# Kernel optimization log

Hardware: AMD Instinct MI355X
Metric: run time of the kernel (lower is better)

The kernel has to match this reference:

```python
import jax, jax.numpy as jnp
import numpy as np

S = 1024      # flattened hierarchical sequence length
D = 1024      # n_embd
H = 16        # n_head
HD = D // H   # head dim (64)
NL = 6        # n_layer
DFF = 4 * D
EPS = 1.1920929e-07  # torch rms_norm default eps (float32 machine eps)


def setup_inputs() -> dict:
    key = jax.random.key(0)
    ks = jax.random.split(key, 12)
    s = 0.02
    return {
        "x": jax.random.normal(ks[0], (1, S, D), jnp.float32),
        "Wq": jax.random.normal(ks[1], (NL, D, D), jnp.float32) * s,
        "Wk": jax.random.normal(ks[2], (NL, D, D), jnp.float32) * s,
        "Wv": jax.random.normal(ks[3], (NL, D, D), jnp.float32) * s,
        "Wo": jax.random.normal(ks[4], (NL, D, D), jnp.float32) * s,
        "lamb": jnp.full((NL,), 0.5, jnp.float32),
        "lambdas": jnp.tile(jnp.array([1.0, 0.0], jnp.float32), (NL, 1)),
        "Wfc": jax.random.normal(ks[5], (NL, DFF, D), jnp.float32) * s,
        "Wp": jax.random.normal(ks[6], (NL, D, DFF), jnp.float32) * s,
        "levels": jax.random.randint(ks[7], (S,), 0, 3, jnp.int32),
        "sample_idx": jnp.sort(jax.random.randint(ks[8], (S,), 0, 8, jnp.int32)),
    }


def rms(t):
    return t * jax.lax.rsqrt(jnp.mean(t * t, axis=-1, keepdims=True) + EPS)


def rope(t):
    # t: [B, T, H, hd]; torch-style half-split rotary
    hd = t.shape[-1]
    d = hd // 2
    inv = 1.0 / (10000.0 ** (jnp.arange(0, hd, 2, dtype=jnp.float32) / hd))
    fr = jnp.outer(jnp.arange(t.shape[1], dtype=jnp.float32), inv)  # [T, d]
    cos = jnp.cos(fr)[None, :, None, :]
    sin = jnp.sin(fr)[None, :, None, :]
    x1, x2 = t[..., :d], t[..., d:]
    return jnp.concatenate([x1 * cos + x2 * sin, -x1 * sin + x2 * cos], axis=-1)


def markov_mask(levels, sample_idx):
    # allowed(q,kv) = causal & same-sample & NOT(levels[kv]==0 and a level-0
    # token exists strictly between kv and q). Equivalent to the torch
    # markov_causal_mask, computed via a cumsum instead of torch.any.
    n = levels.shape[0]
    pos = jnp.arange(n)
    causal = pos[:, None] >= pos[None, :]
    same = sample_idx[:, None] == sample_idx[None, :]
    c = jnp.cumsum((levels == 0).astype(jnp.int32))
    cpad = jnp.concatenate([jnp.zeros((1,), jnp.int32), c])  # cpad[i]=#l0 in [0,i)
    # count of level-0 tokens at positions p with kv < p < q
    cnt = cpad[pos[:, None]] - cpad[pos[None, :] + 1]
    markov = (levels[None, :] == 0) & (cnt > 0)
    return causal & same & ~markov


def reference(x, Wq, Wk, Wv, Wo, lamb, lambdas, Wfc, Wp, levels, sample_idx):
    mask = markov_mask(levels, sample_idx)[None, None]  # [1,1,S,S]
    scale = HD ** -0.5
    neg = jnp.float32(-1e30)

    x = rms(x)          # norm of the hierarchical-trajectory embedding
    x0 = x
    v1 = None
    for i in range(NL):
        xl = lambdas[i, 0] * x + lambdas[i, 1] * x0
        xn = rms(xl)
        B, T = xn.shape[0], xn.shape[1]
        q = (xn @ Wq[i].T).reshape(B, T, H, HD)
        k = (xn @ Wk[i].T).reshape(B, T, H, HD)
        v = (xn @ Wv[i].T).reshape(B, T, H, HD)
        if v1 is None:
            v1 = v
        v = (1.0 - lamb[i]) * v + lamb[i] * v1   # value residual
        q, k = rms(q), rms(k)                    # QK RMSNorm
        q, k = rope(q), rope(k)
        scores = jnp.einsum("bqhd,bkhd->bhqk", q, k) * scale
        scores = jnp.where(mask, scores, neg)
        p = jax.nn.softmax(scores, axis=-1)
        y = jnp.einsum("bhqk,bkhd->bqhd", p, v).reshape(B, T, D)
        x = xl + y @ Wo[i].T
        h = rms(x) @ Wfc[i].T
        h = jnp.square(jax.nn.relu(h))           # relu(x)^2 activation
        x = x + h @ Wp[i].T
    return rms(x)
```

## Files before the change

### kernel.cpp

```cpp
#include <hip/hip_runtime.h>

#define SQ 1024
#define DM 1024
#define NH 16
#define HD 64
#define NL 6
#define DFF 4096
#define EPS 1.1920929e-07f

typedef __attribute__((ext_vector_type(8))) short short8;
typedef __attribute__((ext_vector_type(4))) float floatx4;
typedef __attribute__((address_space(1))) const unsigned int GU32;
typedef __attribute__((address_space(3))) unsigned int LU32;

__device__ __forceinline__ unsigned short f2b(float f) {
    union { float f; unsigned int u; } x; x.f = f;
    unsigned int r = x.u + 0x7fffu + ((x.u >> 16) & 1u);
    return (unsigned short)(r >> 16);
}

__device__ __forceinline__ float wsum(float v) {
#pragma unroll
    for (int m = 32; m >= 1; m >>= 1) v += __shfl_xor(v, m, 64);
    return v;
}
__device__ __forceinline__ float bsum(float v) {
    __shared__ float sh[4];
    v = wsum(v);
    __syncthreads();
    if ((threadIdx.x & 63) == 0) sh[threadIdx.x >> 6] = v;
    __syncthreads();
    return sh[0] + sh[1] + sh[2] + sh[3];
}

__global__ void convert_all(const float* __restrict__ s0, const float* __restrict__ s1,
                            const float* __restrict__ s2, const float* __restrict__ s3,
                            const float* __restrict__ s4, const float* __restrict__ s5,
                            unsigned short* __restrict__ d0, unsigned short* __restrict__ d1,
                            unsigned short* __restrict__ d2, unsigned short* __restrict__ d3,
                            unsigned short* __restrict__ d4, unsigned short* __restrict__ d5) {
    int bid = blockIdx.x;
    const float* src; unsigned short* dst; long base;
    if (bid < 3072)        { src = s0; dst = d0; base = (long)bid * 512; }
    else if (bid < 6144)   { src = s1; dst = d1; base = (long)(bid - 3072) * 512; }
    else if (bid < 9216)   { src = s2; dst = d2; base = (long)(bid - 6144) * 512; }
    else if (bid < 12288)  { src = s3; dst = d3; base = (long)(bid - 9216) * 512; }
    else if (bid < 24576)  { src = s4; dst = d4; base = (long)(bid - 12288) * 512; }
    else                   { src = s5; dst = d5; base = (long)(bid - 24576) * 512; }
    long i0 = base + threadIdx.x;
#pragma unroll
    for (int u = 0; u < 2; ++u) {
        long i = i0 + u * 256;
        float4 v = ((const float4*)src)[i];
        ushort4 o;
        o.x = f2b(v.x); o.y = f2b(v.y); o.z = f2b(v.z); o.w = f2b(v.w);
        ((ushort4*)dst)[i] = o;
    }
}

__global__ void build_rope(float2* __restrict__ tab) {
    int i = blockIdx.x * 256 + threadIdx.x;
    int s = i >> 5, d = i & 31;
    float invf = expf(-((float)(2 * d) / (float)HD) * 9.210340371976184f);
    float fr = (float)s * invf;
    tab[i] = make_float2(cosf(fr), sinf(fr));
}

__global__ void scan_levels(const int* __restrict__ levels, int* __restrict__ cpad) {
    __shared__ int sh[SQ];
    int t = threadIdx.x;
    sh[t] = (levels[t] == 0) ? 1 : 0;
    __syncthreads();
    for (int off = 1; off < SQ; off <<= 1) {
        int v = (t >= off) ? sh[t - off] : 0;
        __syncthreads();
        sh[t] += v;
        __syncthreads();
    }
    cpad[t + 1] = sh[t];
    if (t == 0) cpad[0] = 0;
}

__global__ void build_mask_bits(const int* __restrict__ levels, const int* __restrict__ sidx,
                                const int* __restrict__ cpad, unsigned long long* __restrict__ mb) {
    int i = blockIdx.x * 256 + threadIdx.x;
    int q = i >> 10, k = i & 1023;
    bool causal = q >= k;
    bool same = sidx[q] == sidx[k];
    int cnt = cpad[q] - cpad[k + 1];
    bool markov = (levels[k] == 0) && (cnt > 0);
    bool pred = causal && same && !markov;
    unsigned long long bal = __ballot(pred);
    if ((threadIdx.x & 63) == 0) mb[(size_t)q * 16 + (k >> 6)] = bal;
}

__global__ void rms0(const float* __restrict__ xin, const float* __restrict__ lam2,
                     float* __restrict__ x0, float* __restrict__ xl,
                     unsigned short* __restrict__ xnb) {
    int row = blockIdx.x, t = threadIdx.x;
    float l0 = lam2[0], l1 = lam2[1];
    const float* rp = xin + (size_t)row * DM;
    float v[4]; float ss = 0.f;
#pragma unroll
    for (int j = 0; j < 4; ++j) { v[j] = rp[t + j * 256]; ss += v[j] * v[j]; }
    ss = bsum(ss);
    float inv = rsqrtf(ss / (float)DM + EPS);
    float coef = l0 + l1;
    float w[4]; float ss2 = 0.f;
#pragma unroll
    for (int j = 0; j < 4; ++j) {
        float r = v[j] * inv;
        x0[(size_t)row * DM + t + j * 256] = r;
        w[j] = coef * r;
        ss2 += w[j] * w[j];
    }
    ss2 = bsum(ss2);
    float inv2 = rsqrtf(ss2 / (float)DM + EPS);
#pragma unroll
    for (int j = 0; j < 4; ++j) {
        size_t idx = (size_t)row * DM + t + j * 256;
        xl[idx] = w[j];
        xnb[idx] = f2b(w[j] * inv2);
    }
}

__global__ __launch_bounds__(256, 2)
void gemm_qkv(const unsigned short* __restrict__ A,
              const unsigned short* __restrict__ B0,
              long long sB,
              unsigned short* __restrict__ qb, unsigned short* __restrict__ kb,
              float* __restrict__ vf,
              const float2* __restrict__ rope) {
    constexpr int BM = 64, BN = 128, BK = 32;
    __shared__ unsigned short As[BM * BK];
    __shared__ unsigned short Bs[BN * BK];
    int t = threadIdx.x, wave = t >> 6, lane = t & 63;
    int m0 = blockIdx.y * BM, n0 = blockIdx.x * BN;
    int z = blockIdx.z;
    const unsigned short* Bb = B0 + (size_t)z * sB;
    int r = lane & 15, q4 = lane >> 4;
    int sr = lane >> 2, sseg = lane & 3;
    int wmo = (wave >> 1) * 32, wno = (wave & 1) * 64;

    floatx4 acc[2][4] = {};
    for (int k0 = 0; k0 < DM; k0 += BK) {
        {
            int c = wave;
            const unsigned short* g = A + (size_t)(m0 + c * 16 + sr) * DM + k0 + sseg * 8;
            __builtin_amdgcn_global_load_lds((GU32*)g, (LU32*)(As + c * 512), 16, 0, 0);
        }
#pragma unroll
        for (int j = 0; j < 2; ++j) {
            int c = wave * 2 + j;
            const unsigned short* g = Bb + (size_t)(n0 + c * 16 + sr) * DM + k0 + sseg * 8;
            __builtin_amdgcn_global_load_lds((GU32*)g, (LU32*)(Bs + c * 512), 16, 0, 0);
        }
        __syncthreads();
        short8 af[2], bfr[4];
#pragma unroll
        for (int mi = 0; mi < 2; ++mi)
            af[mi] = *(const short8*)(As + (wmo + mi * 16 + r) * BK + q4 * 8);
#pragma unroll
        for (int ni = 0; ni < 4; ++ni)
            bfr[ni] = *(const short8*)(Bs + (wno + ni * 16 + r) * BK + q4 * 8);
#pragma unroll
        for (int mi = 0; mi < 2; ++mi)
#pragma unroll
            for (int ni = 0; ni < 4; ++ni)
                acc[mi][ni] = __builtin_amdgcn_mfma_f32_16x16x32_bf16(af[mi], bfr[ni], acc[mi][ni], 0, 0, 0);
        __syncthreads();
    }

    if (z == 2) {
#pragma unroll
        for (int mi = 0; mi < 2; ++mi)
#pragma unroll
            for (int ni = 0; ni < 4; ++ni)
#pragma unroll
                for (int j = 0; j < 4; ++j)
                    vf[(size_t)(m0 + wmo + mi * 16 + q4 * 4 + j) * DM + n0 + wno + ni * 16 + r] = acc[mi][ni][j];
        return;
    }
    unsigned short* dst = z ? kb : qb;
#pragma unroll
    for (int mi = 0; mi < 2; ++mi) {
#pragma unroll
        for (int j = 0; j < 4; ++j) {
            int row = m0 + wmo + mi * 16 + q4 * 4 + j;
            float v0 = acc[mi][0][j], v1 = acc[mi][1][j], v2 = acc[mi][2][j], v3 = acc[mi][3][j];
            float ss = v0 * v0 + v1 * v1 + v2 * v2 + v3 * v3;
#pragma unroll
            for (int d = 1; d < 16; d <<= 1) ss += __shfl_xor(ss, d, 64);
            float inv = rsqrtf(ss * (1.f / 64.f) + EPS);
            v0 *= inv; v1 *= inv; v2 *= inv; v3 *= inv;
            float2 t0 = rope[row * 32 + r];
            float2 t1 = rope[row * 32 + 16 + r];
            size_t rb = (size_t)row * DM + n0 + wno + r;
            dst[rb]      = f2b(v0 * t0.x + v2 * t0.y);
            dst[rb + 16] = f2b(v1 * t1.x + v3 * t1.y);
            dst[rb + 32] = f2b(v2 * t0.x - v0 * t0.y);
            dst[rb + 48] = f2b(v3 * t1.x - v1 * t1.y);
        }
    }
}

__global__ void v_post(const float* __restrict__ vf, float* __restrict__ v1,
                       unsigned short* __restrict__ vt, const float* __restrict__ lambp,
                       int first) {
    __shared__ unsigned short tile[64 * 65];
    int b = blockIdx.x;
    int t = threadIdx.x;
    int ts = b >> 4, tc = b & 15;
    float l = lambp[0];
#pragma unroll
    for (int j = 0; j < 16; ++j) {
        int idx = j * 256 + t;
        int s = idx >> 6, c = idx & 63;
        size_t gi = (size_t)(ts * 64 + s) * DM + tc * 64 + c;
        float val = vf[gi];
        float v1v;
        if (first) { v1[gi] = val; v1v = val; } else v1v = v1[gi];
        tile[c * 65 + s] = f2b((1.f - l) * val + l * v1v);
    }
    __syncthreads();
#pragma unroll
    for (int j = 0; j < 16; ++j) {
        int idx = j * 256 + t;
        int c = idx >> 6, s = idx & 63;
        vt[(size_t)(tc * 64 + c) * SQ + ts * 64 + s] = tile[c * 65 + s];
    }
}

__global__ __launch_bounds__(64)
void flash_attn(const unsigned short* __restrict__ qb, const unsigned short* __restrict__ kb,
                const unsigned short* __restrict__ vt, const unsigned long long* __restrict__ mb,
                unsigned short* __restrict__ yb) {
    __shared__ unsigned short Ps[16 * 64];
    int lane = threadIdx.x;
    int qt = blockIdx.x & 63, h = blockIdx.x >> 6;
    int q0 = qt * 16;
    int r = lane & 15, q4 = lane >> 4;
    const unsigned short* qp = qb + (size_t)(q0 + r) * DM + h * HD + q4 * 8;
    short8 aq0 = *(const short8*)qp;
    short8 aq1 = *(const short8*)(qp + 32);
    floatx4 o[4] = {};
    float m[4] = {-1e30f, -1e30f, -1e30f, -1e30f};
    float l[4] = {0.f, 0.f, 0.f, 0.f};
    int nk = (qt >> 2) + 1;
    for (int kt = 0; kt < nk; ++kt) {
        int k0 = kt * 64;
        unsigned long long mw[4];
#pragma unroll
        for (int j = 0; j < 4; ++j) mw[j] = mb[(size_t)(q0 + q4 * 4 + j) * 16 + kt];
        unsigned long long any = mw[0] | mw[1] | mw[2] | mw[3];
        if (__ballot(any != 0ull) == 0ull) continue;
        short8 bk[4][2], bv[4][2];
#pragma unroll
        for (int ni = 0; ni < 4; ++ni) {
            const unsigned short* kp = kb + (size_t)(k0 + ni * 16 + r) * DM + h * HD + q4 * 8;
            bk[ni][0] = *(const short8*)kp;
            bk[ni][1] = *(const short8*)(kp + 32);
            const unsigned short* vp = vt + (size_t)(h * HD + ni * 16 + r) * SQ + k0 + q4 * 8;
            bv[ni][0] = *(const short8*)vp;
            bv[ni][1] = *(const short8*)(vp + 32);
        }
        float sm[4][4];
#pragma unroll
        for (int ni = 0; ni < 4; ++ni) {
            floatx4 z = {};
            z = __builtin_amdgcn_mfma_f32_16x16x32_bf16(aq0, bk[ni][0], z, 0, 0, 0);
            z = __builtin_amdgcn_mfma_f32_16x16x32_bf16(aq1, bk[ni][1], z, 0, 0, 0);
#pragma unroll
            for (int j = 0; j < 4; ++j) {
                float sv = z[j] * 0.125f;
                bool bit = (mw[j] >> (ni * 16 + r)) & 1ull;
                sm[ni][j] = bit ? sv : -__builtin_inff();
            }
        }
        float alpha[4];
#pragma unroll
        for (int j = 0; j < 4; ++j) {
            float v = fmaxf(fmaxf(sm[0][j], sm[1][j]), fmaxf(sm[2][j], sm[3][j]));
#pragma unroll
            for (int d = 1; d < 16; d <<= 1) v = fmaxf(v, __shfl_xor(v, d, 64));
            float mn = fmaxf(m[j], v);
            alpha[j] = __expf(m[j] - mn);
            m[j] = mn;
        }
        float p[4][4];
        float rs[4] = {0.f, 0.f, 0.f, 0.f};
#pragma unroll
        for (int ni = 0; ni < 4; ++ni)
#pragma unroll
            for (int j = 0; j < 4; ++j) {
                p[ni][j] = __expf(sm[ni][j] - m[j]);
                rs[j] += p[ni][j];
            }
#pragma unroll
        for (int j = 0; j < 4; ++j) {
            float v = rs[j];
#pragma unroll
            for (int d = 1; d < 16; d <<= 1) v += __shfl_xor(v, d, 64);
            l[j] = l[j] * alpha[j] + v;
        }
#pragma unroll
        for (int ni = 0; ni < 4; ++ni)
#pragma unroll
            for (int j = 0; j < 4; ++j) {
                o[ni][j] *= alpha[j];
                Ps[(q4 * 4 + j) * 64 + ni * 16 + r] = f2b(p[ni][j]);
            }
        short8 ap0 = *(const short8*)(Ps + r * 64 + q4 * 8);
        short8 ap1 = *(const short8*)(Ps + r * 64 + 32 + q4 * 8);
#pragma unroll
        for (int ni = 0; ni < 4; ++ni) {
            o[ni] = __builtin_amdgcn_mfma_f32_16x16x32_bf16(ap0, bv[ni][0], o[ni], 0, 0, 0);
            o[ni] = __builtin_amdgcn_mfma_f32_16x16x32_bf16(ap1, bv[ni][1], o[ni], 0, 0, 0);
        }
    }
#pragma unroll
    for (int j = 0; j < 4; ++j) l[j] = 1.f / l[j];
#pragma unroll
    for (int ni = 0; ni < 4; ++ni)
#pragma unroll
        for (int j = 0; j < 4; ++j)
            yb[(size_t)(q0 + q4 * 4 + j) * DM + h * HD + ni * 16 + r] = f2b(o[ni][j] * l[j]);
}

template<int BM, int BN>
__global__ __launch_bounds__(256, 2)
void gemm_t(const unsigned short* __restrict__ A, int lda, long long sA,
            const unsigned short* __restrict__ B, int ldb, long long sB,
            float* Cf, unsigned short* Cb, int ldc, long long sC,
            const float* __restrict__ addsrc, int ldadd,
            int K, float scale, int act) {
    constexpr int BK = 32;
    constexpr int MI = BM / 32, NI = BN / 32;
    constexpr int CA = BM / 16, CB = BN / 16;
    constexpr int CAW = CA / 4, CBW = CB / 4;
    __shared__ unsigned short As[BM * BK];
    __shared__ unsigned short Bs[BN * BK];

    int t = threadIdx.x;
    int wave = t >> 6, lane = t & 63;
    int m0 = blockIdx.y * BM, n0 = blockIdx.x * BN;
    int z = blockIdx.z;
    const unsigned short* Ab = A + (size_t)z * sA;
    const unsigned short* Bb = B + (size_t)z * sB;

    int r = lane & 15, q4 = lane >> 4;
    int sr = lane >> 2, sseg = lane & 3;
    int wmo = (wave >> 1) * (BM / 2);
    int wno = (wave & 1) * (BN / 2);

    floatx4 acc[MI][NI] = {};

    for (int k0 = 0; k0 < K; k0 += BK) {
#pragma unroll
        for (int j = 0; j < CAW; ++j) {
            int c = wave * CAW + j;
            const unsigned short* g = Ab + (size_t)(m0 + c * 16 + sr) * lda + k0 + sseg * 8;
            __builtin_amdgcn_global_load_lds((GU32*)g, (LU32*)(As + c * 512), 16, 0, 0);
        }
#pragma unroll
        for (int j = 0; j < CBW; ++j) {
            int c = wave * CBW + j;
            const unsigned short* g = Bb + (size_t)(n0 + c * 16 + sr) * ldb + k0 + sseg * 8;
            __builtin_amdgcn_global_load_lds((GU32*)g, (LU32*)(Bs + c * 512), 16, 0, 0);
        }
        __syncthreads();

        short8 af[MI], bfr[NI];
#pragma unroll
        for (int mi = 0; mi < MI; ++mi)
            af[mi] = *(const short8*)(As + (wmo + mi * 16 + r) * BK + q4 * 8);
#pragma unroll
        for (int ni = 0; ni < NI; ++ni)
            bfr[ni] = *(const short8*)(Bs + (wno + ni * 16 + r) * BK + q4 * 8);
#pragma unroll
        for (int mi = 0; mi < MI; ++mi)
#pragma unroll
            for (int ni = 0; ni < NI; ++ni)
                acc[mi][ni] = __builtin_amdgcn_mfma_f32_16x16x32_bf16(af[mi], bfr[ni], acc[mi][ni], 0, 0, 0);
        __syncthreads();
    }

    size_t cz = (size_t)z * sC;
#pragma unroll
    for (int mi = 0; mi < MI; ++mi) {
#pragma unroll
        for (int ni = 0; ni < NI; ++ni) {
            int col = n0 + wno + ni * 16 + r;
#pragma unroll
            for (int j = 0; j < 4; ++j) {
                int row = m0 + wmo + mi * 16 + q4 * 4 + j;
                float v = acc[mi][ni][j] * scale;
                if (addsrc) v += addsrc[(size_t)row * ldadd + col];
                if (act == 1) { v = fmaxf(v, 0.f); v = v * v; }
                if (Cf) Cf[cz + (size_t)row * ldc + col] = v;
                if (Cb) Cb[cz + (size_t)row * ldc + col] = f2b(v);
            }
        }
    }
}

__global__ void wo_rms(const float* __restrict__ xl, const float* __restrict__ pp,
                       float* __restrict__ x, unsigned short* __restrict__ xhb) {
    int row = blockIdx.x, t = threadIdx.x;
    const long n = (long)SQ * DM;
    size_t base = (size_t)row * DM;
    float a[4]; float ss = 0.f;
#pragma unroll
    for (int j = 0; j < 4; ++j) {
        size_t idx = base + t + j * 256;
        float v = xl[idx] + pp[idx] + pp[idx + n];
        x[idx] = v;
        a[j] = v; ss += v * v;
    }
    ss = bsum(ss);
    float inv = rsqrtf(ss / (float)DM + EPS);
#pragma unroll
    for (int j = 0; j < 4; ++j)
        xhb[base + t + j * 256] = f2b(a[j] * inv);
}

__global__ void proj_reduce_xlrms(const float* __restrict__ x, const float* __restrict__ pp,
                                  const float* __restrict__ x0, const float* __restrict__ lam2,
                                  float* __restrict__ xl, unsigned short* __restrict__ xnb,
                                  float* __restrict__ out, int last) {
    int row = blockIdx.x, t = threadIdx.x;
    const long n = (long)SQ * DM;
    size_t base = (size_t)row * DM;
    float l0 = 0.f, l1 = 0.f;
    if (!last) { l0 = lam2[0]; l1 = lam2[1]; }
    float a[4]; float ss = 0.f;
#pragma unroll
    for (int j = 0; j < 4; ++j) {
        size_t idx = base + t + j * 256;
        float v = x[idx] + pp[idx] + pp[idx + n] + pp[idx + 2 * n] + pp[idx + 3 * n];
        if (!last) { v = l0 * v + l1 * x0[idx]; xl[idx] = v; }
        a[j] = v; ss += v * v;
    }
    ss = bsum(ss);
    float inv = rsqrtf(ss / (float)DM + EPS);
#pragma unroll
    for (int j = 0; j < 4; ++j) {
        size_t idx = base + t + j * 256;
        if (last) out[idx] = a[j] * inv;
        else xnb[idx] = f2b(a[j] * inv);
    }
}

extern "C" void kernel_launch(void* const* d_in, const int* in_sizes, int n_in,
                              void* d_out, int out_size, void* d_ws, size_t ws_size,
                              hipStream_t stream) {
    const float* x_in    = (const float*)d_in[0];
    const float* Wq      = (const float*)d_in[1];
    const float* Wk      = (const float*)d_in[2];
    const float* Wv      = (const float*)d_in[3];
    const float* Wo      = (const float*)d_in[4];
    const float* lamb    = (const float*)d_in[5];
    const float* lambdas = (const float*)d_in[6];
    const float* Wfc     = (const float*)d_in[7];
    const float* Wp      = (const float*)d_in[8];
    const int*   levels  = (const int*)d_in[9];
    const int*   sidx    = (const int*)d_in[10];
    float* out = (float*)d_out;

    char* ws = (char*)d_ws;
    size_t off = 0;
    auto alloc = [&](size_t b) { void* p = ws + off; off = (off + b + 255) & ~(size_t)255; return p; };

    unsigned short* wq_b  = (unsigned short*)alloc((size_t)NL * DM * DM * 2);
    unsigned short* wk_b  = (unsigned short*)alloc((size_t)NL * DM * DM * 2);
    unsigned short* wv_b  = (unsigned short*)alloc((size_t)NL * DM * DM * 2);
    unsigned short* wo_b  = (unsigned short*)alloc((size_t)NL * DM * DM * 2);
    unsigned short* wfc_b = (unsigned short*)alloc((size_t)NL * DFF * DM * 2);
    unsigned short* wp_b  = (unsigned short*)alloc((size_t)NL * DM * DFF * 2);
    int* cpad             = (int*)alloc((SQ + 1) * 4);
    unsigned long long* mb = (unsigned long long*)alloc((size_t)SQ * 16 * 8);
    float2* rope          = (float2*)alloc((size_t)SQ * 32 * 8);
    float* x    = (float*)alloc((size_t)SQ * DM * 4);
    float* x0   = (float*)alloc((size_t)SQ * DM * 4);
    float* xl   = (float*)alloc((size_t)SQ * DM * 4);
    float* vf   = (float*)alloc((size_t)SQ * DM * 4);
    float* v1   = (float*)alloc((size_t)SQ * DM * 4);
    float* pp   = (float*)alloc((size_t)4 * SQ * DM * 4);
    unsigned short* xn_b = (unsigned short*)alloc((size_t)SQ * DM * 2);
    unsigned short* qb   = (unsigned short*)alloc((size_t)SQ * DM * 2);
    unsigned short* kb   = (unsigned short*)alloc((size_t)SQ * DM * 2);
    unsigned short* vt   = (unsigned short*)alloc((size_t)SQ * DM * 2);
    unsigned short* y_b  = (unsigned short*)alloc((size_t)SQ * DM * 2);
    unsigned short* xh_b = (unsigned short*)alloc((size_t)SQ * DM * 2);
    unsigned short* h_b  = (unsigned short*)alloc((size_t)SQ * DFF * 2);

    if (off > ws_size) return;

    const long long WSTRIDE = (long long)NL * DM * DM;
    const long long XSTRIDE = (long long)SQ * DM;

    convert_all<<<36864, 256, 0, stream>>>(Wq, Wk, Wv, Wo, Wfc, Wp,
                                           wq_b, wk_b, wv_b, wo_b, wfc_b, wp_b);

    scan_levels<<<1, 1024, 0, stream>>>(levels, cpad);
    build_mask_bits<<<4096, 256, 0, stream>>>(levels, sidx, cpad, mb);
    build_rope<<<128, 256, 0, stream>>>(rope);

    rms0<<<SQ, 256, 0, stream>>>(x_in, lambdas, x0, xl, xn_b);

    for (int i = 0; i < NL; ++i) {
        gemm_qkv<<<dim3(8, 16, 3), 256, 0, stream>>>(
            xn_b, wq_b + (size_t)i * DM * DM, WSTRIDE, qb, kb, vf, rope);

        v_post<<<256, 256, 0, stream>>>(vf, v1, vt, lamb + i, (i == 0) ? 1 : 0);

        flash_attn<<<1024, 64, 0, stream>>>(qb, kb, vt, mb, y_b);

        gemm_t<64, 64><<<dim3(16, 16, 2), 256, 0, stream>>>(
            y_b, DM, 512, wo_b + (size_t)i * DM * DM, DM, 512,
            pp, nullptr, DM, XSTRIDE, nullptr, 0, 512, 1.f, 0);
        wo_rms<<<SQ, 256, 0, stream>>>(xl, pp, x, xh_b);

        gemm_t<128, 64><<<dim3(64, 8, 1), 256, 0, stream>>>(
            xh_b, DM, 0, wfc_b + (size_t)i * DFF * DM, DM, 0,
            nullptr, h_b, DFF, 0, nullptr, 0, DM, 1.f, 1);
        gemm_t<128, 64><<<dim3(16, 8, 4), 256, 0, stream>>>(
            h_b, DFF, 1024, wp_b + (size_t)i * DM * DFF, DFF, 1024,
            pp, nullptr, DM, XSTRIDE, nullptr, 0, 1024, 1.f, 0);
        proj_reduce_xlrms<<<SQ, 256, 0, stream>>>(
            x, pp, x0, (i < NL - 1) ? (lambdas + 2 * (i + 1)) : nullptr,
            xl, xn_b, out, (i == NL - 1) ? 1 : 0);
    }
}
```

Measured before the change: 1.027 ms.

## Double-buffer GEMM LDS tiles, fuse value post-processing into QKV GEMM, widen conversion

Both GEMM kernels now double-buffer their LDS tiles, so the global-to-LDS load for the next K step is issued before the MFMAs on the current tile. This is meant to overlap memory latency with compute and removes one barrier per iteration. The separate v_post kernel is folded into the QKV GEMM epilogue, which applies the value residual and transposes through an LDS tile, removing the fp32 vf round trip and one launch per layer. The weight conversion kernel also handles 8 elements per thread with 16-byte stores. In exchange, LDS use per block roughly doubles, which may lower occupancy.

New measurement: 1.061 ms. 1.03x slower.

```diff
diff --git a/kernel.cpp b/kernel.cpp
--- a/kernel.cpp
+++ b/kernel.cpp
@@ -41,20 +41,24 @@
                             unsigned short* __restrict__ d4, unsigned short* __restrict__ d5) {
     int bid = blockIdx.x;
     const float* src; unsigned short* dst; long base;
-    if (bid < 3072)        { src = s0; dst = d0; base = (long)bid * 512; }
-    else if (bid < 6144)   { src = s1; dst = d1; base = (long)(bid - 3072) * 512; }
-    else if (bid < 9216)   { src = s2; dst = d2; base = (long)(bid - 6144) * 512; }
-    else if (bid < 12288)  { src = s3; dst = d3; base = (long)(bid - 9216) * 512; }
-    else if (bid < 24576)  { src = s4; dst = d4; base = (long)(bid - 12288) * 512; }
-    else                   { src = s5; dst = d5; base = (long)(bid - 24576) * 512; }
+    if (bid < 1536)        { src = s0; dst = d0; base = (long)bid * 512; }
+    else if (bid < 3072)   { src = s1; dst = d1; base = (long)(bid - 1536) * 512; }
+    else if (bid < 4608)   { src = s2; dst = d2; base = (long)(bid - 3072) * 512; }
+    else if (bid < 6144)   { src = s3; dst = d3; base = (long)(bid - 4608) * 512; }
+    else if (bid < 12288)  { src = s4; dst = d4; base = (long)(bid - 6144) * 512; }
+    else                   { src = s5; dst = d5; base = (long)(bid - 12288) * 512; }
     long i0 = base + threadIdx.x;
 #pragma unroll
     for (int u = 0; u < 2; ++u) {
         long i = i0 + u * 256;
-        float4 v = ((const float4*)src)[i];
-        ushort4 o;
-        o.x = f2b(v.x); o.y = f2b(v.y); o.z = f2b(v.z); o.w = f2b(v.w);
-        ((ushort4*)dst)[i] = o;
+        float4 a = ((const float4*)src)[2 * i];
+        float4 b = ((const float4*)src)[2 * i + 1];
+        short8 o;
+        o[0] = (short)f2b(a.x); o[1] = (short)f2b(a.y);
+        o[2] = (short)f2b(a.z); o[3] = (short)f2b(a.w);
+        o[4] = (short)f2b(b.x); o[5] = (short)f2b(b.y);
+        o[6] = (short)f2b(b.z); o[7] = (short)f2b(b.w);
+        *(short8*)(dst + i * 8) = o;
     }
 }
 
@@ -129,11 +133,13 @@
               const unsigned short* __restrict__ B0,
               long long sB,
               unsigned short* __restrict__ qb, unsigned short* __restrict__ kb,
-              float* __restrict__ vf,
-              const float2* __restrict__ rope) {
+              float* __restrict__ v1, unsigned short* __restrict__ vt,
+              const float2* __restrict__ rope,
+              const float* __restrict__ lambp, int first) {
     constexpr int BM = 64, BN = 128, BK = 32;
-    __shared__ unsigned short As[BM * BK];
-    __shared__ unsigned short Bs[BN * BK];
+    __shared__ unsigned short As[2][BM * BK];
+    __shared__ unsigned short Bs[2][BN * BK];
+    __shared__ unsigned short vtile[128 * 72];
     int t = threadIdx.x, wave = t >> 6, lane = t & 63;
     int m0 = blockIdx.y * BM, n0 = blockIdx.x * BN;
     int z = blockIdx.z;
@@ -143,91 +149,98 @@
     int wmo = (wave >> 1) * 32, wno = (wave & 1) * 64;
 
     floatx4 acc[2][4] = {};
+
+    {
+        const unsigned short* g = A + (size_t)(m0 + wave * 16 + sr) * DM + sseg * 8;
+        __builtin_amdgcn_global_load_lds((GU32*)g, (LU32*)(&As[0][wave * 512]), 16, 0, 0);
+    }
+#pragma unroll
+    for (int j = 0; j < 2; ++j) {
+        int c = wave * 2 + j;
+        const unsigned short* g = Bb + (size_t)(n0 + c * 16 + sr) * DM + sseg * 8;
+        __builtin_amdgcn_global_load_lds((GU32*)g, (LU32*)(&Bs[0][c * 512]), 16, 0, 0);
+    }
+    __syncthreads();
+
+    int cur = 0;
     for (int k0 = 0; k0 < DM; k0 += BK) {
-        {
-            int c = wave;
-            const unsigned short* g = A + (size_t)(m0 + c * 16 + sr) * DM + k0 + sseg * 8;
-            __builtin_amdgcn_global_load_lds((GU32*)g, (LU32*)(As + c * 512), 16, 0, 0);
-        }
-#pragma unroll
-        for (int j = 0; j < 2; ++j) {
-            int c = wave * 2 + j;
-            const unsigned short* g = Bb + (size_t)(n0 + c * 16 + sr) * DM + k0 + sseg * 8;
-            __builtin_amdgcn_global_load_lds((GU32*)g, (LU32*)(Bs + c * 512), 16, 0, 0);
-        }
-        __syncthreads();
+        int kn = k0 + BK;
+        if (kn < DM) {
+            {
+                const unsigned short* g = A + (size_t)(m0 + wave * 16 + sr) * DM + kn + sseg * 8;
+                __builtin_amdgcn_global_load_lds((GU32*)g, (LU32*)(&As[cur ^ 1][wave * 512]), 16, 0, 0);
+            }
+#pragma unroll
+            for (int j = 0; j < 2; ++j) {
+                int c = wave * 2 + j;
+                const unsigned short* g = Bb + (size_t)(n0 + c * 16 + sr) * DM + kn + sseg * 8;
+                __builtin_amdgcn_global_load_lds((GU32*)g, (LU32*)(&Bs[cur ^ 1][c * 512]), 16, 0, 0);
+            }
+        }
         short8 af[2], bfr[4];
 #pragma unroll
         for (int mi = 0; mi < 2; ++mi)
-            af[mi] = *(const short8*)(As + (wmo + mi * 16 + r) * BK + q4 * 8);
+            af[mi] = *(const short8*)(&As[cur][(wmo + mi * 16 + r) * BK + q4 * 8]);
 #pragma unroll
         for (int ni = 0; ni < 4; ++ni)
-            bfr[ni] = *(const short8*)(Bs + (wno + ni * 16 + r) * BK + q4 * 8);
+            bfr[ni] = *(const short8*)(&Bs[cur][(wno + ni * 16 + r) * BK + q4 * 8]);
 #pragma unroll
         for (int mi = 0; mi < 2; ++mi)
 #pragma unroll
             for (int ni = 0; ni < 4; ++ni)
                 acc[mi][ni] = __builtin_amdgcn_mfma_f32_16x16x32_bf16(af[mi], bfr[ni], acc[mi][ni], 0, 0, 0);
         __syncthreads();
+        cur ^= 1;
     }
 
     if (z == 2) {
+        float l = lambp[0];
 #pragma unroll
         for (int mi = 0; mi < 2; ++mi)
 #pragma unroll
             for (int ni = 0; ni < 4; ++ni)
 #pragma unroll
-                for (int j = 0; j < 4; ++j)
-                    vf[(size_t)(m0 + wmo + mi * 16 + q4 * 4 + j) * DM + n0 + wno + ni * 16 + r] = acc[mi][ni][j];
+                for (int j = 0; j < 4; ++j) {
+                    int row = m0 + wmo + mi * 16 + q4 * 4 + j;
+                    int col = n0 + wno + ni * 16 + r;
+                    float val = acc[mi][ni][j];
+                    size_t gi = (size_t)row * DM + col;
+                    float v1v;
+                    if (first) { v1[gi] = val; v1v = val; } else v1v = v1[gi];
+                    vtile[(col - n0) * 72 + (row - m0)] = f2b((1.f - l) * val + l * v1v);
+                }
+        __syncthreads();
+#pragma unroll
+        for (int jj = 0; jj < 4; ++jj) {
+            int idx = jj * 256 + t;
+            int cr = idx >> 3;
+            int seg = idx & 7;
+            short8 o = *(const short8*)(&vtile[cr * 72 + seg * 8]);
+            *(short8*)(vt + (size_t)(n0 + cr) * SQ + m0 + seg * 8) = o;
+        }
         return;
     }
+
     unsigned short* dst = z ? kb : qb;
 #pragma unroll
     for (int mi = 0; mi < 2; ++mi) {
 #pragma unroll
         for (int j = 0; j < 4; ++j) {
             int row = m0 + wmo + mi * 16 + q4 * 4 + j;
-            float v0 = acc[mi][0][j], v1 = acc[mi][1][j], v2 = acc[mi][2][j], v3 = acc[mi][3][j];
-            float ss = v0 * v0 + v1 * v1 + v2 * v2 + v3 * v3;
+            float v0 = acc[mi][0][j], v1x = acc[mi][1][j], v2 = acc[mi][2][j], v3 = acc[mi][3][j];
+            float ss = v0 * v0 + v1x * v1x + v2 * v2 + v3 * v3;
 #pragma unroll
             for (int d = 1; d < 16; d <<= 1) ss += __shfl_xor(ss, d, 64);
             float inv = rsqrtf(ss * (1.f / 64.f) + EPS);
-            v0 *= inv; v1 *= inv; v2 *= inv; v3 *= inv;
+            v0 *= inv; v1x *= inv; v2 *= inv; v3 *= inv;
             float2 t0 = rope[row * 32 + r];
             float2 t1 = rope[row * 32 + 16 + r];
             size_t rb = (size_t)row * DM + n0 + wno + r;
             dst[rb]      = f2b(v0 * t0.x + v2 * t0.y);
-            dst[rb + 16] = f2b(v1 * t1.x + v3 * t1.y);
+            dst[rb + 16] = f2b(v1x * t1.x + v3 * t1.y);
             dst[rb + 32] = f2b(v2 * t0.x - v0 * t0.y);
-            dst[rb + 48] = f2b(v3 * t1.x - v1 * t1.y);
-        }
-    }
-}
-
-__global__ void v_post(const float* __restrict__ vf, float* __restrict__ v1,
-                       unsigned short* __restrict__ vt, const float* __restrict__ lambp,
-                       int first) {
-    __shared__ unsigned short tile[64 * 65];
-    int b = blockIdx.x;
-    int t = threadIdx.x;
-    int ts = b >> 4, tc = b & 15;
-    float l = lambp[0];
-#pragma unroll
-    for (int j = 0; j < 16; ++j) {
-        int idx = j * 256 + t;
-        int s = idx >> 6, c = idx & 63;
-        size_t gi = (size_t)(ts * 64 + s) * DM + tc * 64 + c;
-        float val = vf[gi];
-        float v1v;
-        if (first) { v1[gi] = val; v1v = val; } else v1v = v1[gi];
-        tile[c * 65 + s] = f2b((1.f - l) * val + l * v1v);
-    }
-    __syncthreads();
-#pragma unroll
-    for (int j = 0; j < 16; ++j) {
-        int idx = j * 256 + t;
-        int c = idx >> 6, s = idx & 63;
-        vt[(size_t)(tc * 64 + c) * SQ + ts * 64 + s] = tile[c * 65 + s];
+            dst[rb + 48] = f2b(v3 * t1.x - v1x * t1.y);
+        }
     }
 }
 
@@ -336,10 +349,9 @@
             int K, float scale, int act) {
     constexpr int BK = 32;
     constexpr int MI = BM / 32, NI = BN / 32;
-    constexpr int CA = BM / 16, CB = BN / 16;
-    constexpr int CAW = CA / 4, CBW = CB / 4;
-    __shared__ unsigned short As[BM * BK];
-    __shared__ unsigned short Bs[BN * BK];
+    constexpr int CAW = BM / 64, CBW = BN / 64;
+    __shared__ unsigned short As[2][BM * BK];
+    __shared__ unsigned short Bs[2][BN * BK];
 
     int t = threadIdx.x;
     int wave = t >> 6, lane = t & 63;
@@ -355,34 +367,51 @@
 
     floatx4 acc[MI][NI] = {};
 
+#pragma unroll
+    for (int j = 0; j < CAW; ++j) {
+        int c = wave * CAW + j;
+        const unsigned short* g = Ab + (size_t)(m0 + c * 16 + sr) * lda + sseg * 8;
+        __builtin_amdgcn_global_load_lds((GU32*)g, (LU32*)(&As[0][c * 512]), 16, 0, 0);
+    }
+#pragma unroll
+    for (int j = 0; j < CBW; ++j) {
+        int c = wave * CBW + j;
+        const unsigned short* g = Bb + (size_t)(n0 + c * 16 + sr) * ldb + sseg * 8;
+        __builtin_amdgcn_global_load_lds((GU32*)g, (LU32*)(&Bs[0][c * 512]), 16, 0, 0);
+    }
+    __syncthreads();
+
+    int cur = 0;
     for (int k0 = 0; k0 < K; k0 += BK) {
-#pragma unroll
-        for (int j = 0; j < CAW; ++j) {
-            int c = wave * CAW + j;
-            const unsigned short* g = Ab + (size_t)(m0 + c * 16 + sr) * lda + k0 + sseg * 8;
-            __builtin_amdgcn_global_load_lds((GU32*)g, (LU32*)(As + c * 512), 16, 0, 0);
-        }
-#pragma unroll
-        for (int j = 0; j < CBW; ++j) {
-            int c = wave * CBW + j;
-            const unsigned short* g = Bb + (size_t)(n0 + c * 16 + sr) * ldb + k0 + sseg * 8;
-            __builtin_amdgcn_global_load_lds((GU32*)g, (LU32*)(Bs + c * 512), 16, 0, 0);
-        }
-        __syncthreads();
-
+        int kn = k0 + BK;
+        if (kn < K) {
+#pragma unroll
+            for (int j = 0; j < CAW; ++j) {
+                int c = wave * CAW + j;
+                const unsigned short* g = Ab + (size_t)(m0 + c * 16 + sr) * lda + kn + sseg * 8;
+                __builtin_amdgcn_global_load_lds((GU32*)g, (LU32*)(&As[cur ^ 1][c * 512]), 16, 0, 0);
+            }
+#pragma unroll
+            for (int j = 0; j < CBW; ++j) {
+                int c = wave * CBW + j;
+                const unsigned short* g = Bb + (size_t)(n0 + c * 16 + sr) * ldb + kn + sseg * 8;
+                __builtin_amdgcn_global_load_lds((GU32*)g, (LU32*)(&Bs[cur ^ 1][c * 512]), 16, 0, 0);
+            }
+        }
         short8 af[MI], bfr[NI];
 #pragma unroll
         for (int mi = 0; mi < MI; ++mi)
-            af[mi] = *(const short8*)(As + (wmo + mi * 16 + r) * BK + q4 * 8);
+            af[mi] = *(const short8*)(&As[cur][(wmo + mi * 16 + r) * BK + q4 * 8]);
 #pragma unroll
         for (int ni = 0; ni < NI; ++ni)
-            bfr[ni] = *(const short8*)(Bs + (wno + ni * 16 + r) * BK + q4 * 8);
+            bfr[ni] = *(const short8*)(&Bs[cur][(wno + ni * 16 + r) * BK + q4 * 8]);
 #pragma unroll
         for (int mi = 0; mi < MI; ++mi)
 #pragma unroll
             for (int ni = 0; ni < NI; ++ni)
                 acc[mi][ni] = __builtin_amdgcn_mfma_f32_16x16x32_bf16(af[mi], bfr[ni], acc[mi][ni], 0, 0, 0);
         __syncthreads();
+        cur ^= 1;
     }
 
     size_t cz = (size_t)z * sC;
@@ -483,7 +512,6 @@
     float* x    = (float*)alloc((size_t)SQ * DM * 4);
     float* x0   = (float*)alloc((size_t)SQ * DM * 4);
     float* xl   = (float*)alloc((size_t)SQ * DM * 4);
-    float* vf   = (float*)alloc((size_t)SQ * DM * 4);
     float* v1   = (float*)alloc((size_t)SQ * DM * 4);
     float* pp   = (float*)alloc((size_t)4 * SQ * DM * 4);
     unsigned short* xn_b = (unsigned short*)alloc((size_t)SQ * DM * 2);
@@ -499,7 +527,7 @@
     const long long WSTRIDE = (long long)NL * DM * DM;
     const long long XSTRIDE = (long long)SQ * DM;
 
-    convert_all<<<36864, 256, 0, stream>>>(Wq, Wk, Wv, Wo, Wfc, Wp,
+    convert_all<<<18432, 256, 0, stream>>>(Wq, Wk, Wv, Wo, Wfc, Wp,
                                            wq_b, wk_b, wv_b, wo_b, wfc_b, wp_b);
 
     scan_levels<<<1, 1024, 0, stream>>>(levels, cpad);
@@ -510,9 +538,8 @@
 
     for (int i = 0; i < NL; ++i) {
         gemm_qkv<<<dim3(8, 16, 3), 256, 0, stream>>>(
-            xn_b, wq_b + (size_t)i * DM * DM, WSTRIDE, qb, kb, vf, rope);
-
-        v_post<<<256, 256, 0, stream>>>(vf, v1, vt, lamb + i, (i == 0) ? 1 : 0);
+            xn_b, wq_b + (size_t)i * DM * DM, WSTRIDE, qb, kb, v1, vt, rope,
+            lamb + i, (i == 0) ? 1 : 0);
 
         flash_attn<<<1024, 64, 0, stream>>>(qb, kb, vt, mb, y_b);
 
```
